# Kernel optimization log

Measured on AMD Instinct MI355X. Metric: run time of the kernel, lower is better.

## Reference

```python
import jax, jax.numpy as jnp
import numpy as np

B = 65536       # number of segments (molecules/graphs) = max(batch_indices[0]) + 1
N = 1048576     # nodes per eye
IN_NF, R_OUT, C_OUT = 64, 128, 128
BRAIN_IN, BRAIN_H, BRAIN_OUT = 256, 256, 128


def setup_inputs() -> dict:
    key = jax.random.key(0)
    ks = jax.random.split(key, 16)
    f = jax.random.normal
    s_in = 1.0 / np.sqrt(IN_NF)
    s_r = 1.0 / np.sqrt(R_OUT)
    s_b = 1.0 / np.sqrt(BRAIN_IN)
    s_h = 1.0 / np.sqrt(BRAIN_H)
    return {
        "x0": f(ks[0], (N, IN_NF), jnp.float32),
        "x1": f(ks[1], (N, IN_NF), jnp.float32),
        "idx0": jax.random.randint(ks[2], (N,), 0, B, dtype=jnp.int32),
        "idx1": jax.random.randint(ks[3], (N,), 0, B, dtype=jnp.int32),
        "Wr0": f(ks[4], (IN_NF, R_OUT), jnp.float32) * s_in,
        "br0": jnp.zeros((R_OUT,), jnp.float32),
        "Wc0": f(ks[5], (R_OUT, C_OUT), jnp.float32) * s_r,
        "bc0": jnp.zeros((C_OUT,), jnp.float32),
        "Wr1": f(ks[6], (IN_NF, R_OUT), jnp.float32) * s_in,
        "br1": jnp.zeros((R_OUT,), jnp.float32),
        "Wc1": f(ks[7], (R_OUT, C_OUT), jnp.float32) * s_r,
        "bc1": jnp.zeros((C_OUT,), jnp.float32),
        "Wb1": f(ks[8], (BRAIN_IN, BRAIN_H), jnp.float32) * s_b,
        "bb1": jnp.zeros((BRAIN_H,), jnp.float32),
        "Wb2": f(ks[9], (BRAIN_H, BRAIN_OUT), jnp.float32) * s_h,
        "bb2": jnp.zeros((BRAIN_OUT,), jnp.float32),
    }


def _eye(x, idx, Wr, br, Wc, bc):
    # linear + relu per node: [N, r_out]
    h = jax.nn.relu(x @ Wr + br)
    # scatter-mean over segments -> [B, r_out]; empty segments get 0 (matches
    # torch_scatter mean and the original zero-padding up to maxlen)
    s = jax.ops.segment_sum(h, idx, num_segments=B)
    cnt = jax.ops.segment_sum(jnp.ones((h.shape[0],), h.dtype), idx, num_segments=B)
    mean = s / jnp.maximum(cnt, 1.0)[:, None]
    # per-graph linear + relu -> [B, c_out]
    return jax.nn.relu(mean @ Wc + bc)


def reference(x0, x1, idx0, idx1, Wr0, br0, Wc0, bc0, Wr1, br1, Wc1, bc1, Wb1, bb1, Wb2, bb2):
    e0 = _eye(x0, idx0, Wr0, br0, Wc0, bc0)   # [B, 128]
    e1 = _eye(x1, idx1, Wr1, br1, Wc1, bc1)   # [B, 128]
    z = jnp.concatenate([e0, e1], axis=1)      # [B, 256]
    h = jax.nn.relu(z @ Wb1 + bb1)             # [B, 256]
    return h @ Wb2 + bb2                       # [B, 128]
```

## Files before the change

### kernel.cpp

```cpp
#include <hip/hip_runtime.h>
#include <hip/hip_bf16.h>

#define B_SEG 65536
#define N_NODES 1048576

typedef _Float16 f16;
typedef __attribute__((ext_vector_type(8))) _Float16 f16x8;
typedef __attribute__((ext_vector_type(2))) __fp16 fp16x2;
typedef __attribute__((ext_vector_type(4))) float f32x4;
typedef unsigned short u16;

union F16x8 { f16x8 v; fp16x2 h2[4]; };

#define MFMA16(a, b, acc) __builtin_amdgcn_mfma_f32_16x16x32_f16((a), (b), (acc), 0, 0, 0)

__global__ __launch_bounds__(256) void histo_part(const int* __restrict__ idx0,
        const int* __restrict__ idx1, int* __restrict__ cnt0, int* __restrict__ cnt1,
        u16* __restrict__ rank0, u16* __restrict__ rank1) {
    int part  = blockIdx.x & 7;
    int chunk = blockIdx.x >> 3;
    int base4 = chunk * (N_NODES / 256 / 4);
    for (int g = base4 + threadIdx.x; g < base4 + N_NODES / 256 / 4; g += 256) {
        int4 s0 = ((const int4*)idx0)[g];
        int i = g * 4;
        if ((s0.x >> 13) == part) { int p = atomicAdd(&cnt0[s0.x], 1); rank0[i]     = (u16)p; }
        if ((s0.y >> 13) == part) { int p = atomicAdd(&cnt0[s0.y], 1); rank0[i + 1] = (u16)p; }
        if ((s0.z >> 13) == part) { int p = atomicAdd(&cnt0[s0.z], 1); rank0[i + 2] = (u16)p; }
        if ((s0.w >> 13) == part) { int p = atomicAdd(&cnt0[s0.w], 1); rank0[i + 3] = (u16)p; }
        int4 s1 = ((const int4*)idx1)[g];
        if ((s1.x >> 13) == part) { int p = atomicAdd(&cnt1[s1.x], 1); rank1[i]     = (u16)p; }
        if ((s1.y >> 13) == part) { int p = atomicAdd(&cnt1[s1.y], 1); rank1[i + 1] = (u16)p; }
        if ((s1.z >> 13) == part) { int p = atomicAdd(&cnt1[s1.z], 1); rank1[i + 2] = (u16)p; }
        if ((s1.w >> 13) == part) { int p = atomicAdd(&cnt1[s1.w], 1); rank1[i + 3] = (u16)p; }
    }
}

__global__ __launch_bounds__(256) void scan1(const int* __restrict__ cnt, int* __restrict__ bsum) {
    int b = blockIdx.x, t = threadIdx.x;
    int4 v = ((const int4*)cnt)[b * 256 + t];
    int s = v.x + v.y + v.z + v.w;
    for (int d = 1; d < 64; d <<= 1) s += __shfl_xor(s, d);
    __shared__ int ws4[4];
    if ((t & 63) == 0) ws4[t >> 6] = s;
    __syncthreads();
    if (t == 0) bsum[b] = ws4[0] + ws4[1] + ws4[2] + ws4[3];
}

__global__ __launch_bounds__(128) void scan2(int* __restrict__ bsum) {
    int t = threadIdx.x, lane = t & 63;
    int v = bsum[t];
    int s = v;
    for (int d = 1; d < 64; d <<= 1) { int u = __shfl_up(s, d); if (lane >= d) s += u; }
    bsum[t] = s - v;
}

__global__ __launch_bounds__(256) void scan3(const int* __restrict__ cnt, const int* __restrict__ bsum,
                                             int* __restrict__ off0, int* __restrict__ off1) {
    int b = blockIdx.x, t = threadIdx.x;
    int4 v = ((const int4*)cnt)[b * 256 + t];
    int local = v.x + v.y + v.z + v.w;
    int lane = t & 63, w = t >> 6;
    int s = local;
    for (int d = 1; d < 64; d <<= 1) { int u = __shfl_up(s, d); if (lane >= d) s += u; }
    __shared__ int wsum[4];
    if (lane == 63) wsum[w] = s;
    __syncthreads();
    int carry = bsum[b];
    for (int i = 0; i < w; ++i) carry += wsum[i];
    int ex = carry + s - local;
    int* off = (b < 64) ? off0 : off1;
    int gi = (b & 63) * 1024 + t * 4;
    off[gi] = ex; ex += v.x; off[gi + 1] = ex; ex += v.y; off[gi + 2] = ex; ex += v.z; off[gi + 3] = ex;
    if (b == 0 && t == 0) { off0[B_SEG] = N_NODES; off1[B_SEG] = N_NODES; }
}

__global__ __launch_bounds__(256) void fill_prep(const int* __restrict__ idx0,
        const int* __restrict__ idx1, const u16* __restrict__ rank0, const u16* __restrict__ rank1,
        const int* __restrict__ off0, const int* __restrict__ off1,
        int* __restrict__ ord0, int* __restrict__ ord1,
        const float* __restrict__ Wc0, const float* __restrict__ Wc1,
        const float* __restrict__ Wb1, const float* __restrict__ Wb2,
        f16* __restrict__ T0, f16* __restrict__ T1, f16* __restrict__ T2, f16* __restrict__ T3) {
    if (blockIdx.x < 2048) {
        const int stride = 2048 * 256;
        for (int g = blockIdx.x * 256 + threadIdx.x; g < N_NODES / 4; g += stride) {
            int4 s0 = ((const int4*)idx0)[g];
            ushort4 r0 = ((const ushort4*)rank0)[g];
            int i = g * 4;
            ord0[off0[s0.x] + r0.x] = i;
            ord0[off0[s0.y] + r0.y] = i + 1;
            ord0[off0[s0.z] + r0.z] = i + 2;
            ord0[off0[s0.w] + r0.w] = i + 3;
            int4 s1 = ((const int4*)idx1)[g];
            ushort4 r1 = ((const ushort4*)rank1)[g];
            ord1[off1[s1.x] + r1.x] = i;
            ord1[off1[s1.y] + r1.y] = i + 1;
            ord1[off1[s1.z] + r1.z] = i + 2;
            ord1[off1[s1.w] + r1.w] = i + 3;
        }
    } else {
        int b = blockIdx.x - 2048, t = threadIdx.x;
        if (b < 64)        { int i = b * 256 + t;         T0[i] = (f16)Wc0[(i & 127) * 128 + (i >> 7)]; }
        else if (b < 128)  { int i = (b - 64) * 256 + t;  T1[i] = (f16)Wc1[(i & 127) * 128 + (i >> 7)]; }
        else if (b < 384)  { int i = (b - 128) * 256 + t; T2[i] = (f16)Wb1[(i & 255) * 256 + (i >> 8)]; }
        else               { int i = (b - 384) * 256 + t; T3[i] = (f16)Wb2[(i & 255) * 128 + (i >> 8)]; }
    }
}

#define SEGS_PER_WAVE 8
__global__ __launch_bounds__(256, 3) void eye_means_mfma(
        const float* __restrict__ xA, const float* __restrict__ WrA, const float* __restrict__ brA,
        const int* __restrict__ offA, const int* __restrict__ ordA, f16* __restrict__ meansA,
        const float* __restrict__ xB, const float* __restrict__ WrB, const float* __restrict__ brB,
        const int* __restrict__ offB, const int* __restrict__ ordB, f16* __restrict__ meansB) {
    const float *x, *Wr, *br; const int *off, *ord; f16* means;
    if (blockIdx.y == 0) { x = xA; Wr = WrA; br = brA; off = offA; ord = ordA; means = meansA; }
    else                 { x = xB; Wr = WrB; br = brB; off = offB; ord = ordB; means = meansB; }

    int lane = threadIdx.x & 63;
    int wid  = blockIdx.x * 4 + (threadIdx.x >> 6);
    int c  = lane & 15;
    int kq = lane >> 4;

    f16x8 bfr[8][2];
    float rbias[8];
    #pragma unroll
    for (int g = 0; g < 8; ++g) {
        #pragma unroll
        for (int h = 0; h < 2; ++h)
            #pragma unroll
            for (int j = 0; j < 8; ++j)
                bfr[g][h][j] = (f16)Wr[(size_t)(h * 32 + kq * 8 + j) * 128 + g * 16 + c];
        rbias[g] = br[g * 16 + c];
    }

    int s_begin = wid * SEGS_PER_WAVE;
    int offv  = off[s_begin + ((lane <= 8) ? lane : 8)];
    int base0 = __shfl(offv, 0);
    int nxtv  = __shfl(offv, (lane < 8) ? (lane + 1) : 8);
    int szl   = nxtv - offv;

    int ov0 = ord[base0 + lane];
    int ov1 = ord[base0 + 64 + lane];
    int ov2 = ord[base0 + 128 + lane];

    auto node_at = [&](int off_rel, int sz, int r) -> int {
        int e  = off_rel + r;
        int e6 = e & 63;
        int n0 = __shfl(ov0, e6);
        int n1 = __shfl(ov1, e6);
        int n2 = __shfl(ov2, e6);
        int n  = (e < 64) ? n0 : (e < 128) ? n1 : n2;
        if (e >= 192) n = ord[base0 + e];
        return (r < sz) ? n : 0;
    };

    auto loadx = [&](int node, float4& v0, float4& v1, float4& v2, float4& v3) {
        const float* xp = &x[(size_t)node * 64 + kq * 8];
        v0 = *(const float4*)(xp);      v1 = *(const float4*)(xp + 4);
        v2 = *(const float4*)(xp + 32); v3 = *(const float4*)(xp + 36);
    };

    float sum[8];
    #pragma unroll
    for (int g = 0; g < 8; ++g) sum[g] = 0.f;

    float4 ca, cb, cc, cd;
    {
        int sz0 = __shfl(szl, 0);
        loadx(node_at(0, sz0, c), ca, cb, cc, cd);
    }

    #pragma unroll
    for (int s = 0; s < SEGS_PER_WAVE; ++s) {
        int off_rel   = __shfl(offv, s) - base0;
        int sz        = __shfl(szl, s);
        int nb        = (sz + 15) >> 4;
        int off_rel_n = (s < SEGS_PER_WAVE - 1) ? (__shfl(offv, s + 1) - base0) : 0;
        int sz_n      = (s < SEGS_PER_WAVE - 1) ? __shfl(szl, s + 1) : 0;
        size_t mb     = (size_t)(s_begin + s) * 128;

        if (nb == 0) {
            means[mb + (2 * kq + 0) * 16 + c] = (f16)0.f;
            means[mb + (2 * kq + 1) * 16 + c] = (f16)0.f;
            loadx(node_at(off_rel_n, sz_n, c), ca, cb, cc, cd);
            continue;
        }

        for (int b = 0; b < nb; ++b) {
            int nn = (b + 1 < nb) ? node_at(off_rel, sz, (b + 1) * 16 + c)
                                  : node_at(off_rel_n, sz_n, c);
            float4 pa, pb, pc, pd;
            loadx(nn, pa, pb, pc, pd);

            f16x8 A0 = {}, A1 = {};
            if (b * 16 + c < sz) {
                F16x8 u0, u1;
                u0.h2[0] = __builtin_amdgcn_cvt_pkrtz(ca.x, ca.y);
                u0.h2[1] = __builtin_amdgcn_cvt_pkrtz(ca.z, ca.w);
                u0.h2[2] = __builtin_amdgcn_cvt_pkrtz(cb.x, cb.y);
                u0.h2[3] = __builtin_amdgcn_cvt_pkrtz(cb.z, cb.w);
                u1.h2[0] = __builtin_amdgcn_cvt_pkrtz(cc.x, cc.y);
                u1.h2[1] = __builtin_amdgcn_cvt_pkrtz(cc.z, cc.w);
                u1.h2[2] = __builtin_amdgcn_cvt_pkrtz(cd.x, cd.y);
                u1.h2[3] = __builtin_amdgcn_cvt_pkrtz(cd.z, cd.w);
                A0 = u0.v; A1 = u1.v;
            }
            #pragma unroll
            for (int g = 0; g < 8; ++g) {
                f32x4 acc = {0.f, 0.f, 0.f, 0.f};
                acc = MFMA16(A0, bfr[g][0], acc);
                acc = MFMA16(A1, bfr[g][1], acc);
                #pragma unroll
                for (int r = 0; r < 4; ++r)
                    sum[g] += fmaxf(acc[r] + rbias[g], 0.f);
            }
            ca = pa; cb = pb; cc = pc; cd = pd;
        }

        float padc = (float)(nb * 16 - sz);
        float inv  = 1.f / (float)sz;
        #pragma unroll
        for (int g = 0; g < 8; ++g) {
            float v = sum[g];
            v += __shfl_xor(v, 16);
            v += __shfl_xor(v, 32);
            v -= padc * fmaxf(rbias[g], 0.f);
            sum[g] = v * inv;
        }
        means[mb + (2 * kq + 0) * 16 + c] = (f16)sum[2 * kq + 0];
        means[mb + (2 * kq + 1) * 16 + c] = (f16)sum[2 * kq + 1];
        #pragma unroll
        for (int g = 0; g < 8; ++g) sum[g] = 0.f;
    }
}

template<int K, int RELU, int OUT16>
__global__ __launch_bounds__(256) void gemm16(
        const f16* __restrict__ A, const f16* __restrict__ BT,
        const float* __restrict__ bias, void* __restrict__ Cv, int ldc) {
    int lane = threadIdx.x & 63;
    int w = threadIdx.x >> 6;
    int c = lane & 15, kq = lane >> 4;
    int m0 = blockIdx.x * 128 + w * 32;
    int n0 = blockIdx.y * 128;

    f32x4 acc[2][8] = {};
    const f16* arow0 = A + (size_t)(m0 + c) * K + kq * 8;
    const f16* arow1 = arow0 + (size_t)16 * K;
    const f16* brow  = BT + (size_t)(n0 + c) * K + kq * 8;

    #pragma unroll 2
    for (int k0 = 0; k0 < K; k0 += 32) {
        f16x8 a0 = *(const f16x8*)(arow0 + k0);
        f16x8 a1 = *(const f16x8*)(arow1 + k0);
        #pragma unroll
        for (int g = 0; g < 8; ++g) {
            f16x8 bf = *(const f16x8*)(brow + (size_t)g * 16 * K + k0);
            acc[0][g] = MFMA16(a0, bf, acc[0][g]);
            acc[1][g] = MFMA16(a1, bf, acc[1][g]);
        }
    }

    #pragma unroll
    for (int g = 0; g < 8; ++g) {
        float bv = bias[n0 + g * 16 + c];
        #pragma unroll
        for (int ms = 0; ms < 2; ++ms) {
            #pragma unroll
            for (int r = 0; r < 4; ++r) {
                float v = acc[ms][g][r] + bv;
                if (RELU) v = fmaxf(v, 0.f);
                size_t ci = (size_t)(m0 + ms * 16 + kq * 4 + r) * ldc + n0 + g * 16 + c;
                if (OUT16) ((f16*)Cv)[ci] = (f16)v;
                else       ((float*)Cv)[ci] = v;
            }
        }
    }
}

__global__ __launch_bounds__(256) void gemm_wc(
        const f16* __restrict__ M0, const f16* __restrict__ M1,
        const f16* __restrict__ T0, const f16* __restrict__ T1,
        const float* __restrict__ bc0, const float* __restrict__ bc1,
        f16* __restrict__ z) {
    int e = blockIdx.y;
    const f16* A  = e ? M1 : M0;
    const f16* BT = e ? T1 : T0;
    const float* bias = e ? bc1 : bc0;
    int lane = threadIdx.x & 63;
    int w = threadIdx.x >> 6;
    int c = lane & 15, kq = lane >> 4;
    int m0 = blockIdx.x * 128 + w * 32;

    f32x4 acc[2][8] = {};
    const f16* arow0 = A + (size_t)(m0 + c) * 128 + kq * 8;
    const f16* arow1 = arow0 + (size_t)16 * 128;
    const f16* brow  = BT + (size_t)c * 128 + kq * 8;

    #pragma unroll
    for (int k0 = 0; k0 < 128; k0 += 32) {
        f16x8 a0 = *(const f16x8*)(arow0 + k0);
        f16x8 a1 = *(const f16x8*)(arow1 + k0);
        #pragma unroll
        for (int g = 0; g < 8; ++g) {
            f16x8 bf = *(const f16x8*)(brow + (size_t)g * 16 * 128 + k0);
            acc[0][g] = MFMA16(a0, bf, acc[0][g]);
            acc[1][g] = MFMA16(a1, bf, acc[1][g]);
        }
    }

    #pragma unroll
    for (int g = 0; g < 8; ++g) {
        float bv = bias[g * 16 + c];
        #pragma unroll
        for (int ms = 0; ms < 2; ++ms) {
            #pragma unroll
            for (int r = 0; r < 4; ++r) {
                float v = fmaxf(acc[ms][g][r] + bv, 0.f);
                z[(size_t)(m0 + ms * 16 + kq * 4 + r) * 256 + e * 128 + g * 16 + c] = (f16)v;
            }
        }
    }
}

extern "C" void kernel_launch(void* const* d_in, const int* in_sizes, int n_in,
                              void* d_out, int out_size, void* d_ws, size_t ws_size,
                              hipStream_t stream) {
    const float* x0  = (const float*)d_in[0];
    const float* x1  = (const float*)d_in[1];
    const int*   idx0 = (const int*)d_in[2];
    const int*   idx1 = (const int*)d_in[3];
    const float* Wr0 = (const float*)d_in[4];
    const float* br0 = (const float*)d_in[5];
    const float* Wc0 = (const float*)d_in[6];
    const float* bc0 = (const float*)d_in[7];
    const float* Wr1 = (const float*)d_in[8];
    const float* br1 = (const float*)d_in[9];
    const float* Wc1 = (const float*)d_in[10];
    const float* bc1 = (const float*)d_in[11];
    const float* Wb1 = (const float*)d_in[12];
    const float* bb1 = (const float*)d_in[13];
    const float* Wb2 = (const float*)d_in[14];
    const float* bb2 = (const float*)d_in[15];
    float* out = (float*)d_out;

    char* w = (char*)d_ws;
    auto alloc = [&](size_t bytes) { void* p = (void*)w; w += (bytes + 255) & ~(size_t)255; return p; };
    int* cnt0 = (int*)alloc((size_t)B_SEG * 4);
    int* cnt1 = (int*)alloc((size_t)B_SEG * 4);
    int* off0 = (int*)alloc((size_t)(B_SEG + 1) * 4);
    int* off1 = (int*)alloc((size_t)(B_SEG + 1) * 4);
    int* ord0 = (int*)alloc((size_t)(N_NODES + 256) * 4);
    int* ord1 = (int*)alloc((size_t)(N_NODES + 256) * 4);
    u16* rank0 = (u16*)alloc((size_t)N_NODES * 2);
    u16* rank1 = (u16*)alloc((size_t)N_NODES * 2);
    int* bsum = (int*)alloc(128 * 4);
    f16* means0 = (f16*)alloc((size_t)B_SEG * 128 * 2);
    f16* means1 = (f16*)alloc((size_t)B_SEG * 128 * 2);
    f16* z      = (f16*)alloc((size_t)B_SEG * 256 * 2);
    f16* hb     = (f16*)alloc((size_t)B_SEG * 256 * 2);
    f16* T0     = (f16*)alloc((size_t)128 * 128 * 2);
    f16* T1     = (f16*)alloc((size_t)128 * 128 * 2);
    f16* T2     = (f16*)alloc((size_t)256 * 256 * 2);
    f16* T3     = (f16*)alloc((size_t)128 * 256 * 2);

    (void)hipMemsetAsync(cnt0, 0, 2 * (size_t)B_SEG * sizeof(int), stream);
    histo_part<<<2048, 256, 0, stream>>>(idx0, idx1, cnt0, cnt1, rank0, rank1);
    scan1<<<128, 256, 0, stream>>>(cnt0, bsum);
    scan2<<<1, 128, 0, stream>>>(bsum);
    scan3<<<128, 256, 0, stream>>>(cnt0, bsum, off0, off1);
    fill_prep<<<2048 + 512, 256, 0, stream>>>(idx0, idx1, rank0, rank1, off0, off1,
                                              ord0, ord1, Wc0, Wc1, Wb1, Wb2, T0, T1, T2, T3);

    eye_means_mfma<<<dim3(2048, 2), 256, 0, stream>>>(
        x0, Wr0, br0, off0, ord0, means0,
        x1, Wr1, br1, off1, ord1, means1);

    gemm_wc<<<dim3(512, 2), 256, 0, stream>>>(means0, means1, T0, T1, bc0, bc1, z);
    gemm16<256, 1, 1><<<dim3(512, 2), 256, 0, stream>>>(z,  T2, bb1, hb,  256);
    gemm16<256, 0, 0><<<dim3(512, 1), 256, 0, stream>>>(hb, T3, bb2, out, 128);
}
```

Before: 420.4 us.

## Give each segment partition its own rank array to avoid conflicting writes

The histogram kernel now writes ranks into one private u16 array per partition (8 copies per eye) instead of a single shared array. This removes the interleaved 2-byte writes from different blocks into the same cache lines. The fill kernel now uses the same part/chunk block mapping, reads its partition's rank array, and scatters only the nodes that belong to that partition. The cost is an 8x larger rank buffer and extra idx reads in the fill kernel. The partition-sorted scatter into ord may also improve locality of the off and ord accesses.

```diff
diff --git a/kernel.cpp b/kernel.cpp
--- a/kernel.cpp
+++ b/kernel.cpp
@@ -16,22 +16,24 @@
 
 __global__ __launch_bounds__(256) void histo_part(const int* __restrict__ idx0,
         const int* __restrict__ idx1, int* __restrict__ cnt0, int* __restrict__ cnt1,
-        u16* __restrict__ rank0, u16* __restrict__ rank1) {
+        u16* __restrict__ rankp0, u16* __restrict__ rankp1) {
     int part  = blockIdx.x & 7;
     int chunk = blockIdx.x >> 3;
+    u16* r0 = rankp0 + (size_t)part * N_NODES;
+    u16* r1 = rankp1 + (size_t)part * N_NODES;
     int base4 = chunk * (N_NODES / 256 / 4);
     for (int g = base4 + threadIdx.x; g < base4 + N_NODES / 256 / 4; g += 256) {
         int4 s0 = ((const int4*)idx0)[g];
         int i = g * 4;
-        if ((s0.x >> 13) == part) { int p = atomicAdd(&cnt0[s0.x], 1); rank0[i]     = (u16)p; }
-        if ((s0.y >> 13) == part) { int p = atomicAdd(&cnt0[s0.y], 1); rank0[i + 1] = (u16)p; }
-        if ((s0.z >> 13) == part) { int p = atomicAdd(&cnt0[s0.z], 1); rank0[i + 2] = (u16)p; }
-        if ((s0.w >> 13) == part) { int p = atomicAdd(&cnt0[s0.w], 1); rank0[i + 3] = (u16)p; }
+        if ((s0.x >> 13) == part) { int p = atomicAdd(&cnt0[s0.x], 1); r0[i]     = (u16)p; }
+        if ((s0.y >> 13) == part) { int p = atomicAdd(&cnt0[s0.y], 1); r0[i + 1] = (u16)p; }
+        if ((s0.z >> 13) == part) { int p = atomicAdd(&cnt0[s0.z], 1); r0[i + 2] = (u16)p; }
+        if ((s0.w >> 13) == part) { int p = atomicAdd(&cnt0[s0.w], 1); r0[i + 3] = (u16)p; }
         int4 s1 = ((const int4*)idx1)[g];
-        if ((s1.x >> 13) == part) { int p = atomicAdd(&cnt1[s1.x], 1); rank1[i]     = (u16)p; }
-        if ((s1.y >> 13) == part) { int p = atomicAdd(&cnt1[s1.y], 1); rank1[i + 1] = (u16)p; }
-        if ((s1.z >> 13) == part) { int p = atomicAdd(&cnt1[s1.z], 1); rank1[i + 2] = (u16)p; }
-        if ((s1.w >> 13) == part) { int p = atomicAdd(&cnt1[s1.w], 1); rank1[i + 3] = (u16)p; }
+        if ((s1.x >> 13) == part) { int p = atomicAdd(&cnt1[s1.x], 1); r1[i]     = (u16)p; }
+        if ((s1.y >> 13) == part) { int p = atomicAdd(&cnt1[s1.y], 1); r1[i + 1] = (u16)p; }
+        if ((s1.z >> 13) == part) { int p = atomicAdd(&cnt1[s1.z], 1); r1[i + 2] = (u16)p; }
+        if ((s1.w >> 13) == part) { int p = atomicAdd(&cnt1[s1.w], 1); r1[i + 3] = (u16)p; }
     }
 }
 
@@ -75,28 +77,32 @@
 }
 
 __global__ __launch_bounds__(256) void fill_prep(const int* __restrict__ idx0,
-        const int* __restrict__ idx1, const u16* __restrict__ rank0, const u16* __restrict__ rank1,
+        const int* __restrict__ idx1, const u16* __restrict__ rankp0, const u16* __restrict__ rankp1,
         const int* __restrict__ off0, const int* __restrict__ off1,
         int* __restrict__ ord0, int* __restrict__ ord1,
         const float* __restrict__ Wc0, const float* __restrict__ Wc1,
         const float* __restrict__ Wb1, const float* __restrict__ Wb2,
         f16* __restrict__ T0, f16* __restrict__ T1, f16* __restrict__ T2, f16* __restrict__ T3) {
     if (blockIdx.x < 2048) {
-        const int stride = 2048 * 256;
-        for (int g = blockIdx.x * 256 + threadIdx.x; g < N_NODES / 4; g += stride) {
+        int part  = blockIdx.x & 7;
+        int chunk = blockIdx.x >> 3;
+        const u16* r0 = rankp0 + (size_t)part * N_NODES;
+        const u16* r1 = rankp1 + (size_t)part * N_NODES;
+        int base4 = chunk * (N_NODES / 256 / 4);
+        for (int g = base4 + threadIdx.x; g < base4 + N_NODES / 256 / 4; g += 256) {
             int4 s0 = ((const int4*)idx0)[g];
-            ushort4 r0 = ((const ushort4*)rank0)[g];
+            ushort4 q0 = ((const ushort4*)r0)[g];
             int i = g * 4;
-            ord0[off0[s0.x] + r0.x] = i;
-            ord0[off0[s0.y] + r0.y] = i + 1;
-            ord0[off0[s0.z] + r0.z] = i + 2;
-            ord0[off0[s0.w] + r0.w] = i + 3;
+            if ((s0.x >> 13) == part) ord0[off0[s0.x] + q0.x] = i;
+            if ((s0.y >> 13) == part) ord0[off0[s0.y] + q0.y] = i + 1;
+            if ((s0.z >> 13) == part) ord0[off0[s0.z] + q0.z] = i + 2;
+            if ((s0.w >> 13) == part) ord0[off0[s0.w] + q0.w] = i + 3;
             int4 s1 = ((const int4*)idx1)[g];
-            ushort4 r1 = ((const ushort4*)rank1)[g];
-            ord1[off1[s1.x] + r1.x] = i;
-            ord1[off1[s1.y] + r1.y] = i + 1;
-            ord1[off1[s1.z] + r1.z] = i + 2;
-            ord1[off1[s1.w] + r1.w] = i + 3;
+            ushort4 q1 = ((const ushort4*)r1)[g];
+            if ((s1.x >> 13) == part) ord1[off1[s1.x] + q1.x] = i;
+            if ((s1.y >> 13) == part) ord1[off1[s1.y] + q1.y] = i + 1;
+            if ((s1.z >> 13) == part) ord1[off1[s1.z] + q1.z] = i + 2;
+            if ((s1.w >> 13) == part) ord1[off1[s1.w] + q1.w] = i + 3;
         }
     } else {
         int b = blockIdx.x - 2048, t = threadIdx.x;
@@ -353,8 +359,8 @@
     int* off1 = (int*)alloc((size_t)(B_SEG + 1) * 4);
     int* ord0 = (int*)alloc((size_t)(N_NODES + 256) * 4);
     int* ord1 = (int*)alloc((size_t)(N_NODES + 256) * 4);
-    u16* rank0 = (u16*)alloc((size_t)N_NODES * 2);
-    u16* rank1 = (u16*)alloc((size_t)N_NODES * 2);
+    u16* rankp0 = (u16*)alloc((size_t)8 * N_NODES * 2);
+    u16* rankp1 = (u16*)alloc((size_t)8 * N_NODES * 2);
     int* bsum = (int*)alloc(128 * 4);
     f16* means0 = (f16*)alloc((size_t)B_SEG * 128 * 2);
     f16* means1 = (f16*)alloc((size_t)B_SEG * 128 * 2);
@@ -366,11 +372,11 @@
     f16* T3     = (f16*)alloc((size_t)128 * 256 * 2);
 
     (void)hipMemsetAsync(cnt0, 0, 2 * (size_t)B_SEG * sizeof(int), stream);
-    histo_part<<<2048, 256, 0, stream>>>(idx0, idx1, cnt0, cnt1, rank0, rank1);
+    histo_part<<<2048, 256, 0, stream>>>(idx0, idx1, cnt0, cnt1, rankp0, rankp1);
     scan1<<<128, 256, 0, stream>>>(cnt0, bsum);
     scan2<<<1, 128, 0, stream>>>(bsum);
     scan3<<<128, 256, 0, stream>>>(cnt0, bsum, off0, off1);
-    fill_prep<<<2048 + 512, 256, 0, stream>>>(idx0, idx1, rank0, rank1, off0, off1,
+    fill_prep<<<2048 + 512, 256, 0, stream>>>(idx0, idx1, rankp0, rankp1, off0, off1,
                                               ord0, ord1, Wc0, Wc1, Wb1, Wb2, T0, T1, T2, T3);
 
     eye_means_mfma<<<dim3(2048, 2), 256, 0, stream>>>(
```

After: 421.0 us. About the same (+0.1%).
